# Kernel optimization log

Hardware: AMD Instinct MI355X
Metric: run time of the kernel (lower is better)

## Reference

```python
import jax, jax.numpy as jnp
import numpy as np

N_NODES = 100000
N_EDGES = 1600000
IN_DIM, HID_DIM, OUT_DIM = 128, 128, 64


def setup_inputs() -> dict:
    key = jax.random.key(0)
    ks = jax.random.split(key, 5)
    x = jax.random.normal(ks[0], (N_NODES, IN_DIM), dtype=jnp.float32)
    edge_index = jax.random.randint(ks[1], (2, N_EDGES), 0, N_NODES, dtype=jnp.int64)
    W1 = jax.random.normal(ks[2], (IN_DIM, HID_DIM), dtype=jnp.float32) * (1.0 / np.sqrt(IN_DIM))
    b1 = jnp.zeros((HID_DIM,), dtype=jnp.float32)
    W2 = jax.random.normal(ks[3], (HID_DIM, OUT_DIM), dtype=jnp.float32) * (1.0 / np.sqrt(HID_DIM))
    b2 = jnp.zeros((OUT_DIM,), dtype=jnp.float32)
    return {"x": x, "edge_index": edge_index, "W1": W1, "b1": b1, "W2": W2, "b2": b2}


def _gcn_conv(h, row, col, norm, b, n_nodes):
    # h: [N, F] already linearly transformed; message = norm_e * h[src]; scatter-add to dst
    msg = h[row] * norm[:, None]                      # [E+N, F]
    out = jax.ops.segment_sum(msg, col, num_segments=n_nodes)
    return out + b


def reference(x, edge_index, W1, b1, W2, b2):
    n = x.shape[0]
    loops = jnp.arange(n, dtype=edge_index.dtype)
    row = jnp.concatenate([edge_index[0], loops])     # sources (incl. self loops)
    col = jnp.concatenate([edge_index[1], loops])     # targets
    # symmetric normalization: deg over targets with unit edge weights
    deg = jax.ops.segment_sum(jnp.ones_like(col, dtype=x.dtype), col, num_segments=n)
    dinv = jnp.where(deg > 0, jax.lax.rsqrt(jnp.maximum(deg, 1.0)), 0.0)
    norm = dinv[row] * dinv[col]                      # [E+N]
    h = jax.nn.relu(_gcn_conv(x @ W1, row, col, norm, b1, n))
    out = _gcn_conv(h @ W2, row, col, norm, b2, n)
    return out.mean(axis=0)                           # [OUT_DIM]
```

## Files before the change

kernel.cpp:

```cpp
#include <hip/hip_runtime.h>

#define N_NODES 100000
#define N_EDGES 1600000
#define IN_DIM 128
#define HID_DIM 128
#define OUT_DIM 64
#define BKT_SHIFT 7
#define BKT_SIZE 128
#define NBKT ((N_NODES + BKT_SIZE - 1) / BKT_SIZE)
#define B1 256
#define HIST_N (NBKT * B1)
#define HIST_N2 (2 * HIST_N)
#define GEMM_BLKS ((N_NODES + 127) / 128)
#define AGG_BLKS 2048
#define NPW 13

typedef float v2f __attribute__((ext_vector_type(2)));
typedef float v4f __attribute__((ext_vector_type(4)));
typedef short v8s __attribute__((ext_vector_type(8)));

__device__ __forceinline__ int permb(int b) { return ((b & 7) << 5) | (b >> 3); }

__device__ __forceinline__ unsigned int f2bf(float f) {
  unsigned int u = __float_as_uint(f);
  return (u + 0x7FFFu + ((u >> 16) & 1u)) >> 16;
}

template <bool HI>
__device__ __forceinline__ v2f cvt8(unsigned int u) {
  return __builtin_amdgcn_cvt_pk_f32_fp8((int)u, HI);
}

__device__ __forceinline__ void load4(const void* ei, int is64, int half, int base,
                                      int* v) {
  if (is64) {
    const long long* e = (const long long*)ei + (size_t)half * N_EDGES + base;
    longlong2 a = *(const longlong2*)e;
    longlong2 b = *(const longlong2*)(e + 2);
    v[0] = (int)a.x; v[1] = (int)a.y; v[2] = (int)b.x; v[3] = (int)b.y;
  } else {
    const int* e = (const int*)ei + (size_t)half * N_EDGES + base;
    int4 a = *(const int4*)e;
    v[0] = a.x; v[1] = a.y; v[2] = a.z; v[3] = a.w;
  }
}

__device__ __forceinline__ int detect64_block(const unsigned int* ei, int* sh) {
  if (threadIdx.x == 0) *sh = 0;
  __syncthreads();
  if (ei[1 + 2 * threadIdx.x] != 0u) *sh = 1;
  __syncthreads();
  return (*sh == 0) ? 1 : 0;
}

__global__ __launch_bounds__(256) void front_kernel(const float* __restrict__ x,
                                                    const float* __restrict__ W,
                                                    const void* ei,
                                                    unsigned int* __restrict__ G,
                                                    int* hist, float* S) {
  __shared__ __align__(16) char smem[2 * 128 * 136 * 2];
  if (blockIdx.x >= GEMM_BLKS) {
    int* hd = (int*)smem;
    int* hs = hd + NBKT;
    int* sh = hs + NBKT;
    const int hb = blockIdx.x - GEMM_BLKS;
    const int pj = permb(hb);
    if (hb == 0 && threadIdx.x < HID_DIM) S[threadIdx.x] = 0.f;
    const int is64 = detect64_block((const unsigned int*)ei, sh);
    for (int k = threadIdx.x; k < NBKT; k += 256) { hd[k] = 0; hs[k] = 0; }
    __syncthreads();
    for (int g = hb * 256 + threadIdx.x; g < N_EDGES / 4; g += B1 * 256) {
      int r[4], c[4];
      load4(ei, is64, 0, g * 4, r);
      load4(ei, is64, 1, g * 4, c);
#pragma unroll
      for (int k = 0; k < 4; k++) {
        atomicAdd(&hd[c[k] >> BKT_SHIFT], 1);
        atomicAdd(&hs[r[k] >> BKT_SHIFT], 1);
      }
    }
    __syncthreads();
    for (int k = threadIdx.x; k < NBKT; k += 256) {
      hist[k * B1 + pj] = hd[k];
      hist[HIST_N + k * B1 + pj] = hs[k];
    }
    return;
  }
  typedef unsigned short us_row[136];
  us_row* lx = (us_row*)smem;
  us_row* lwt = (us_row*)(smem + 128 * 136 * 2);
  const int t = threadIdx.x;
  const int row0 = blockIdx.x * 128;

  {
    const float4* W4 = (const float4*)W;
    for (int it = 0; it < 16; ++it) {
      int idx = t + 256 * it;
      int k = idx >> 5, c4 = (idx & 31) * 4;
      float4 w = W4[idx];
      lwt[c4 + 0][k] = (unsigned short)f2bf(w.x);
      lwt[c4 + 1][k] = (unsigned short)f2bf(w.y);
      lwt[c4 + 2][k] = (unsigned short)f2bf(w.z);
      lwt[c4 + 3][k] = (unsigned short)f2bf(w.w);
    }
  }
  {
    const float4* x4 = (const float4*)(x + (size_t)row0 * IN_DIM);
    for (int it = 0; it < 16; ++it) {
      int idx = t + 256 * it;
      int r = idx >> 5, kq = (idx & 31) * 4;
      float4 v = make_float4(0.f, 0.f, 0.f, 0.f);
      if (row0 + r < N_NODES) v = x4[idx];
      unsigned int p0 = (f2bf(v.y) << 16) | f2bf(v.x);
      unsigned int p1 = (f2bf(v.w) << 16) | f2bf(v.z);
      *(uint2*)&lx[r][kq] = make_uint2(p0, p1);
    }
  }
  __syncthreads();

  const int lane = t & 63;
  const int wv = t >> 6;
  const int m0 = wv * 32;
  const int lrow = lane & 15;
  const int lk = (lane >> 4) * 8;

  v4f acc[2][8];
#pragma unroll
  for (int si = 0; si < 2; si++)
#pragma unroll
    for (int n = 0; n < 8; n++) acc[si][n] = (v4f){0.f, 0.f, 0.f, 0.f};

#pragma unroll
  for (int kk = 0; kk < 128; kk += 32) {
    v8s a0 = *(const v8s*)&lx[m0 + lrow][kk + lk];
    v8s a1 = *(const v8s*)&lx[m0 + 16 + lrow][kk + lk];
#pragma unroll
    for (int n = 0; n < 8; n++) {
      v8s b = *(const v8s*)&lwt[n * 16 + lrow][kk + lk];
      acc[0][n] = __builtin_amdgcn_mfma_f32_16x16x32_bf16(a0, b, acc[0][n], 0, 0, 0);
      acc[1][n] = __builtin_amdgcn_mfma_f32_16x16x32_bf16(a1, b, acc[1][n], 0, 0, 0);
    }
  }

  unsigned char* G8 = (unsigned char*)G;
#pragma unroll
  for (int si = 0; si < 2; si++)
#pragma unroll
    for (int n = 0; n < 8; n++) {
      int colg = n * 16 + (lane & 15);
#pragma unroll
      for (int i = 0; i < 4; i++) {
        int r = row0 + m0 + si * 16 + (lane >> 4) * 4 + i;
        if (r < N_NODES) {
          float v = acc[si][n][i];
          int pk = __builtin_amdgcn_cvt_pk_fp8_f32(v, v, 0, false);
          G8[(size_t)r * HID_DIM + colg] = (unsigned char)(pk & 0xFF);
        }
      }
    }
}

__global__ void scan1_kernel(int* arr, int* bsum, int n) {
  __shared__ int tmp[256];
  int i = blockIdx.x * 256 + threadIdx.x;
  int v = (i < n) ? arr[i] : 0;
  tmp[threadIdx.x] = v;
  __syncthreads();
  for (int off = 1; off < 256; off <<= 1) {
    int t2 = (threadIdx.x >= off) ? tmp[threadIdx.x - off] : 0;
    __syncthreads();
    tmp[threadIdx.x] += t2;
    __syncthreads();
  }
  if (i < n) arr[i] = tmp[threadIdx.x] - v;
  if (threadIdx.x == 255) bsum[blockIdx.x] = tmp[255];
}

__global__ void scan2_kernel(int* bsum, int nb) {
  __shared__ int tmp[1024];
  const int t = threadIdx.x;
  int v0 = (2 * t < nb) ? bsum[2 * t] : 0;
  int v1 = (2 * t + 1 < nb) ? bsum[2 * t + 1] : 0;
  int s = v0 + v1;
  tmp[t] = s;
  __syncthreads();
  for (int off = 1; off < 1024; off <<= 1) {
    int t2 = (t >= off) ? tmp[t - off] : 0;
    __syncthreads();
    tmp[t] += t2;
    __syncthreads();
  }
  int excl = tmp[t] - s;
  if (2 * t < nb) bsum[2 * t] = excl;
  if (2 * t + 1 < nb) bsum[2 * t + 1] = excl + v0;
}

__global__ __launch_bounds__(256) void scatter_kernel(const void* ei, const int* hist,
                                                      const int* bsum,
                                                      unsigned int* pairs) {
  __shared__ int cd[NBKT], cs[NBKT], sh[1];
  const int is64 = detect64_block((const unsigned int*)ei, sh);
  const int pj = permb(blockIdx.x);
  for (int k = threadIdx.x; k < NBKT; k += 256) {
    cd[k] = hist[k * B1 + pj] + bsum[k];
    cs[k] = hist[HIST_N + k * B1 + pj] + bsum[NBKT + k];
  }
  __syncthreads();
  for (int g = blockIdx.x * 256 + threadIdx.x; g < N_EDGES / 4; g += B1 * 256) {
    int r[4], c[4];
    load4(ei, is64, 0, g * 4, r);
    load4(ei, is64, 1, g * 4, c);
#pragma unroll
    for (int k = 0; k < 4; k++) {
      int pd = atomicAdd(&cd[c[k] >> BKT_SHIFT], 1);
      pairs[pd] = ((unsigned int)(c[k] & (BKT_SIZE - 1)) << 17) | (unsigned int)r[k];
      int ps = atomicAdd(&cs[r[k] >> BKT_SHIFT], 1);
      pairs[ps] = ((unsigned int)(r[k] & (BKT_SIZE - 1)) << 17) | (unsigned int)c[k];
    }
  }
}

__global__ __launch_bounds__(256) void csrA_kernel(const int* hist, const int* bsum,
                                                   const unsigned int* pairs,
                                                   int* rowptr, float* dinv) {
  __shared__ int cnt[BKT_SIZE], sc[BKT_SIZE];
  const int k = blockIdx.x;
  const int base = hist[k * B1] + bsum[k];
  const int end = (k == NBKT - 1) ? N_EDGES : hist[(k + 1) * B1] + bsum[k + 1];
  const int nseg = end - base;
  const int l = threadIdx.x;
  if (l < BKT_SIZE) cnt[l] = 0;
  __syncthreads();
  for (int i = l; i < nseg; i += 256) atomicAdd(&cnt[pairs[base + i] >> 17], 1);
  __syncthreads();
  if (l < BKT_SIZE) sc[l] = cnt[l];
  __syncthreads();
  for (int off = 1; off < BKT_SIZE; off <<= 1) {
    int v = (l < BKT_SIZE && l >= off) ? sc[l - off] : 0;
    __syncthreads();
    if (l < BKT_SIZE) sc[l] += v;
    __syncthreads();
  }
  if (l < BKT_SIZE) {
    int excl = sc[l] - cnt[l];
    int v = k * BKT_SIZE + l;
    if (v < N_NODES) {
      rowptr[v] = base + excl;
      dinv[v] = rsqrtf((float)(cnt[l] + 1));
    }
  }
  if (k == NBKT - 1 && l == 0) rowptr[N_NODES] = N_EDGES;
}

__global__ __launch_bounds__(256) void csrBout_kernel(const int* hist, const int* bsum,
                                                      const unsigned int* pairs,
                                                      const int* __restrict__ rowptr,
                                                      const float* __restrict__ dinv,
                                                      unsigned int* __restrict__ csr,
                                                      float* __restrict__ wacc) {
  if (blockIdx.x < NBKT) {
    __shared__ int cur[BKT_SIZE];
    const int k = blockIdx.x;
    const int base = hist[k * B1] + bsum[k];
    const int end = (k == NBKT - 1) ? N_EDGES : hist[(k + 1) * B1] + bsum[k + 1];
    const int nseg = end - base;
    const int l = threadIdx.x;
    if (l < BKT_SIZE) {
      int v = k * BKT_SIZE + l;
      cur[l] = (v < N_NODES) ? rowptr[v] : 0;
    }
    __syncthreads();
    for (int i = l; i < nseg; i += 256) {
      unsigned int pk = pairs[base + i];
      unsigned int src = pk & 0x1FFFFu;
      int pos = atomicAdd(&cur[pk >> 17], 1);
      unsigned int bits = f2bf(dinv[src]);
      csr[pos] = (bits << 17) | src;
    }
    return;
  }
  __shared__ float fb[BKT_SIZE];
  const int k = blockIdx.x - NBKT;
  const int base = hist[HIST_N + k * B1] + bsum[NBKT + k];
  const int end =
      (k == NBKT - 1) ? 2 * N_EDGES : hist[HIST_N + (k + 1) * B1] + bsum[NBKT + k + 1];
  if (threadIdx.x < BKT_SIZE) fb[threadIdx.x] = 0.f;
  __syncthreads();
  for (int i = base + threadIdx.x; i < end; i += 256) {
    unsigned int pk = pairs[i];
    atomicAdd(&fb[pk >> 17], dinv[pk & 0x1FFFFu]);
  }
  __syncthreads();
  int v = k * BKT_SIZE + threadIdx.x;
  if (threadIdx.x < BKT_SIZE && v < N_NODES) wacc[v] = fb[threadIdx.x];
}

__global__ __launch_bounds__(256) void aggregate_kernel(
    const unsigned int* __restrict__ G, const int* __restrict__ rowptr,
    const unsigned int* __restrict__ csr, const float* __restrict__ dinv,
    const float* __restrict__ wacc, const float* __restrict__ b1,
    float* __restrict__ S) {
  __shared__ float lsw[4][HID_DIM];
  const int lane = threadIdx.x & 63;
  const int wv = threadIdx.x >> 6;
  const int wid = blockIdx.x * 4 + wv;
  const int c0 = wid * NPW;
  const unsigned short* __restrict__ Gu = (const unsigned short*)G;

  int rp = 0;
  float dvv = 0.f, wvv = 0.f;
  {
    const int ci = c0 + lane;
    if (lane <= NPW && ci <= N_NODES) rp = rowptr[ci];
    if (lane < NPW && ci < N_NODES) { dvv = dinv[ci]; wvv = wacc[ci]; }
  }
  const v2f bl = *(const v2f*)&b1[2 * lane];
  v2f s = {0.f, 0.f};
  const int nn = (c0 < N_NODES) ? min(NPW, N_NODES - c0) : 0;

  int sCur = __shfl(rp, 0);
  int eCur = __shfl(rp, 1);
  unsigned int pwNxt = 0;
  unsigned int gsNxt = 0;
  if (nn > 0) {
    if (lane < eCur - sCur) pwNxt = __builtin_nontemporal_load(&csr[sCur + lane]);
    gsNxt = Gu[(unsigned)c0 * 64u + lane];
  }

  for (int k = 0; k < nn; ++k) {
    const int st = sCur;
    const int deg = eCur - sCur;
    unsigned int pw = pwNxt;
    const unsigned int gs = gsNxt;
    const float d = __shfl(dvv, k);
    const float wa = __shfl(wvv, k);
    if (k + 1 < nn) {
      sCur = eCur;
      eCur = __shfl(rp, k + 2);
      pwNxt = 0;
      if (lane < eCur - sCur) pwNxt = __builtin_nontemporal_load(&csr[sCur + lane]);
      gsNxt = Gu[(unsigned)(c0 + k + 1) * 64u + lane];
    }

    v2f a = cvt8<false>(gs) * d;
    int j0 = 0;
    for (;;) {
      const int m = min(64, deg - j0);
      unsigned int gA[8], gB[8];
      float wA[8], wB[8];
#define LD8(gv, wv, base)                                       \
  _Pragma("unroll") for (int t = 0; t < 8; ++t) {               \
    const unsigned int p = __shfl(pw, (base) + t);              \
    wv[t] = __uint_as_float((p >> 17) << 16);                   \
    gv[t] = Gu[(unsigned)(p & 0x1FFFFu) * 64u + lane];          \
  }
#define CONS8(gv, wv)                                           \
  _Pragma("unroll") for (int t = 0; t < 8; ++t) {               \
    a += cvt8<false>(gv[t]) * wv[t];                            \
  }
      LD8(gA, wA, 0)
      int i = 0;
      for (;;) {
        if (i + 8 < m) { LD8(gB, wB, i + 8) }
        CONS8(gA, wA)
        i += 8;
        if (i >= m) break;
        if (i + 8 < m) { LD8(gA, wA, i + 8) }
        CONS8(gB, wB)
        i += 8;
        if (i >= m) break;
      }
#undef LD8
#undef CONS8
      j0 += 64;
      if (j0 >= deg) break;
      pw = 0;
      if (lane < deg - j0) pw = __builtin_nontemporal_load(&csr[st + j0 + lane]);
    }
    const float wc = d * (wa + d);
    s.x += wc * fmaxf(fmaf(d, a.x, bl.x), 0.f);
    s.y += wc * fmaxf(fmaf(d, a.y, bl.y), 0.f);
  }

  lsw[wv][2 * lane + 0] = s.x;
  lsw[wv][2 * lane + 1] = s.y;
  __syncthreads();
  if (threadIdx.x < HID_DIM) {
    const float v = lsw[0][threadIdx.x] + lsw[1][threadIdx.x] +
                    lsw[2][threadIdx.x] + lsw[3][threadIdx.x];
    atomicAdd(&S[threadIdx.x], v);
  }
}

__global__ void finish_kernel(const float* __restrict__ S, const float* __restrict__ W2,
                              const float* __restrict__ b2, float* __restrict__ out) {
  int j = threadIdx.x;
  float acc = 0.f;
  for (int k = 0; k < HID_DIM; k++) acc += S[k] * W2[k * OUT_DIM + j];
  out[j] = acc * (1.0f / N_NODES) + b2[j];
}

extern "C" void kernel_launch(void* const* d_in, const int* in_sizes, int n_in,
                              void* d_out, int out_size, void* d_ws, size_t ws_size,
                              hipStream_t stream) {
  const float* x  = (const float*)d_in[0];
  const void*  ei = d_in[1];
  const float* W1 = (const float*)d_in[2];
  const float* b1 = (const float*)d_in[3];
  const float* W2 = (const float*)d_in[4];
  const float* b2 = (const float*)d_in[5];
  float* out = (float*)d_out;

  char* p = (char*)d_ws;
  size_t off = 0;
  auto alloc = [&](size_t bytes) -> void* {
    void* r = p + off;
    off = (off + bytes + 63) & ~(size_t)63;
    return r;
  };
  int*   hist   = (int*)alloc((size_t)HIST_N2 * 4);
  int*   bsum   = (int*)alloc(2048 * 4);
  unsigned int* pairs = (unsigned int*)alloc((size_t)2 * N_EDGES * 4);
  int*   rowptr = (int*)alloc(((size_t)N_NODES + 1) * 4);
  unsigned int* csr = (unsigned int*)alloc((size_t)N_EDGES * 4);
  float* dinv   = (float*)alloc((size_t)N_NODES * 4);
  float* wacc   = (float*)alloc((size_t)N_NODES * 4);
  float* S      = (float*)alloc(HID_DIM * 4);
  unsigned int* G = (unsigned int*)alloc((size_t)N_NODES * HID_DIM);
  (void)ws_size; (void)n_in; (void)in_sizes; (void)out_size;

  const int NBH = HIST_N2 / 256;

  front_kernel<<<GEMM_BLKS + B1, 256, 0, stream>>>(x, W1, ei, G, hist, S);
  scan1_kernel<<<NBH, 256, 0, stream>>>(hist, bsum, HIST_N2);
  scan2_kernel<<<1, 1024, 0, stream>>>(bsum, NBH);
  scatter_kernel<<<B1, 256, 0, stream>>>(ei, hist, bsum, pairs);
  csrA_kernel<<<NBKT, 256, 0, stream>>>(hist, bsum, pairs, rowptr, dinv);
  csrBout_kernel<<<2 * NBKT, 256, 0, stream>>>(hist, bsum, pairs, rowptr, dinv, csr,
                                               wacc);
  aggregate_kernel<<<AGG_BLKS, 256, 0, stream>>>(G, rowptr, csr, dinv, wacc, b1, S);
  finish_kernel<<<1, 64, 0, stream>>>(S, W2, b2, out);
}
```

Measured before the change: 321.0 us.

## Flatten per-wave edge loop across nodes with 16-wide double-buffered gathers

Replaces the per-node edge loop with a single flat loop over all edges of the wave's 13 nodes. Gathers are issued 16 at a time with double buffering, so loads stay in flight across node boundaries instead of draining at each node's end. Node transitions are detected inside the consume loop, and per-node scalars are made wave-uniform with readfirstlane. This adds branching inside the unrolled consume loop and raises register pressure from the 16-element buffers.

```diff
diff --git a/kernel.cpp b/kernel.cpp
--- a/kernel.cpp
+++ b/kernel.cpp
@@ -29,6 +29,11 @@
 template <bool HI>
 __device__ __forceinline__ v2f cvt8(unsigned int u) {
   return __builtin_amdgcn_cvt_pk_f32_fp8((int)u, HI);
+}
+
+__device__ __forceinline__ int rfl(int v) { return __builtin_amdgcn_readfirstlane(v); }
+__device__ __forceinline__ float rflf(float v) {
+  return __uint_as_float(__builtin_amdgcn_readfirstlane(__float_as_uint(v)));
 }
 
 __device__ __forceinline__ void load4(const void* ei, int is64, int half, int base,
@@ -318,68 +323,85 @@
   v2f s = {0.f, 0.f};
   const int nn = (c0 < N_NODES) ? min(NPW, N_NODES - c0) : 0;
 
-  int sCur = __shfl(rp, 0);
-  int eCur = __shfl(rp, 1);
-  unsigned int pwNxt = 0;
-  unsigned int gsNxt = 0;
   if (nn > 0) {
-    if (lane < eCur - sCur) pwNxt = __builtin_nontemporal_load(&csr[sCur + lane]);
-    gsNxt = Gu[(unsigned)c0 * 64u + lane];
-  }
-
-  for (int k = 0; k < nn; ++k) {
-    const int st = sCur;
-    const int deg = eCur - sCur;
-    unsigned int pw = pwNxt;
-    const unsigned int gs = gsNxt;
-    const float d = __shfl(dvv, k);
-    const float wa = __shfl(wvv, k);
-    if (k + 1 < nn) {
-      sCur = eCur;
-      eCur = __shfl(rp, k + 2);
-      pwNxt = 0;
-      if (lane < eCur - sCur) pwNxt = __builtin_nontemporal_load(&csr[sCur + lane]);
-      gsNxt = Gu[(unsigned)(c0 + k + 1) * 64u + lane];
-    }
-
-    v2f a = cvt8<false>(gs) * d;
-    int j0 = 0;
+    const int eBeg = rfl(__shfl(rp, 0));
+    const int eEnd = rfl(__shfl(rp, nn));
+
+    unsigned int gsA = Gu[(unsigned)c0 * 64u + lane];
+    unsigned int gsB = Gu[(unsigned)(c0 + min(1, nn - 1)) * 64u + lane];
+
+    unsigned int pwCur = 0, pwNxt = 0;
+    {
+      const int idx = eBeg + lane;
+      if (idx < eEnd) pwNxt = __builtin_nontemporal_load(&csr[idx]);
+    }
+
+    int k = 0;
+    float d = 0.f, wa = 0.f;
+    int bEnd = 0;
+    v2f a = {0.f, 0.f};
+
+    auto startNode = [&](int kk) {
+      d = rflf(__shfl(dvv, kk));
+      wa = rflf(__shfl(wvv, kk));
+      bEnd = rfl(__shfl(rp, kk + 1));
+      a = cvt8<false>(gsA) * d;
+      gsA = gsB;
+      gsB = Gu[(unsigned)(c0 + min(kk + 2, nn - 1)) * 64u + lane];
+    };
+    auto finishNode = [&]() {
+      const float wc = d * (wa + d);
+      s.x += wc * fmaxf(fmaf(d, a.x, bl.x), 0.f);
+      s.y += wc * fmaxf(fmaf(d, a.y, bl.y), 0.f);
+      k++;
+      if (k < nn) startNode(k);
+      else bEnd = -1;
+    };
+    auto LOADT = [&](unsigned int(&gb)[16], unsigned int(&wb)[8], int epos) {
+      const int off = (epos - eBeg) & 63;
+      if (off == 0) {
+        pwCur = pwNxt;
+        pwNxt = 0;
+        const int idx = epos + 64 + lane;
+        if (idx < eEnd) pwNxt = __builtin_nontemporal_load(&csr[idx]);
+      }
+      unsigned int wtmp = 0;
+#pragma unroll
+      for (int t = 0; t < 16; ++t) {
+        const unsigned int p = __shfl(pwCur, off + t);
+        gb[t] = Gu[(unsigned)(p & 0x1FFFFu) * 64u + lane];
+        if ((t & 1) == 0) wtmp = (p >> 17) << 16;
+        else wb[t >> 1] = wtmp | (p >> 17);
+      }
+    };
+    auto CONS = [&](const unsigned int(&gb)[16], const unsigned int(&wb)[8],
+                    int epos) {
+#pragma unroll
+      for (int t = 0; t < 16; ++t) {
+        while (k < nn && epos + t == bEnd) finishNode();
+        const float w = ((t & 1) == 0)
+                            ? __uint_as_float(wb[t >> 1] & 0xFFFF0000u)
+                            : __uint_as_float(wb[t >> 1] << 16);
+        a += cvt8<false>(gb[t]) * w;
+      }
+    };
+
+    startNode(0);
+    unsigned int g0[16], g1[16], wp0[8], wq0[8];
+    LOADT(g0, wp0, eBeg);
+    int eC = eBeg;
     for (;;) {
-      const int m = min(64, deg - j0);
-      unsigned int gA[8], gB[8];
-      float wA[8], wB[8];
-#define LD8(gv, wv, base)                                       \
-  _Pragma("unroll") for (int t = 0; t < 8; ++t) {               \
-    const unsigned int p = __shfl(pw, (base) + t);              \
-    wv[t] = __uint_as_float((p >> 17) << 16);                   \
-    gv[t] = Gu[(unsigned)(p & 0x1FFFFu) * 64u + lane];          \
-  }
-#define CONS8(gv, wv)                                           \
-  _Pragma("unroll") for (int t = 0; t < 8; ++t) {               \
-    a += cvt8<false>(gv[t]) * wv[t];                            \
-  }
-      LD8(gA, wA, 0)
-      int i = 0;
-      for (;;) {
-        if (i + 8 < m) { LD8(gB, wB, i + 8) }
-        CONS8(gA, wA)
-        i += 8;
-        if (i >= m) break;
-        if (i + 8 < m) { LD8(gA, wA, i + 8) }
-        CONS8(gB, wB)
-        i += 8;
-        if (i >= m) break;
-      }
-#undef LD8
-#undef CONS8
-      j0 += 64;
-      if (j0 >= deg) break;
-      pw = 0;
-      if (lane < deg - j0) pw = __builtin_nontemporal_load(&csr[st + j0 + lane]);
-    }
-    const float wc = d * (wa + d);
-    s.x += wc * fmaxf(fmaf(d, a.x, bl.x), 0.f);
-    s.y += wc * fmaxf(fmaf(d, a.y, bl.y), 0.f);
+      const int eN = eC + 16;
+      if (eN < eEnd) LOADT(g1, wq0, eN);
+      CONS(g0, wp0, eC);
+      if (eN >= eEnd) break;
+      const int eN2 = eN + 16;
+      if (eN2 < eEnd) LOADT(g0, wp0, eN2);
+      CONS(g1, wq0, eN);
+      if (eN2 >= eEnd) break;
+      eC = eN2;
+    }
+    while (k < nn) finishNode();
   }
 
   lsw[wv][2 * lane + 0] = s.x;
```

Measured after the change: 343.0 us. 1.07x slower.
